# Kernel tuning notes

Measured on AMD Instinct MI355X. Metric: run time of the kernel, lower is better.

The kernel has to match this reference:

```python
import jax, jax.numpy as jnp
import numpy as np

NUM_HEADS = 8
WINDOW = 5


def local_mask(T, w):
    # non-causal band: attend iff |i - j| <= w
    i = jnp.arange(T)
    return jnp.abs(i[:, None] - i[None, :]) <= w


def setup_inputs() -> dict:
    key = jax.random.key(0)
    k1, k2, k3 = jax.random.split(key, 3)
    B, T, S, C = 2, 64, 1024, 512  # batch, frames, spatial (32x32), hidden
    x = jax.random.normal(k1, (B, T * S, C), dtype=jnp.float32)
    W_qkv = jax.random.normal(k2, (C, 3 * C), dtype=jnp.float32) * (C ** -0.5)
    W_out = jax.random.normal(k3, (C, C), dtype=jnp.float32) * (C ** -0.5)
    return {"x": x, "W_qkv": W_qkv, "W_out": W_out, "num_frames": T}


def reference(x, W_qkv, W_out, num_frames):
    B, N, C = x.shape
    H = NUM_HEADS
    hd = C // H
    T = num_frames
    S = N // T
    scale = hd ** -0.5

    qkv = (x @ W_qkv).reshape(B, T, S, 3, H, hd)
    q = qkv[:, :, :, 0]  # [B,T,S,H,hd]
    k = qkv[:, :, :, 1]
    v = qkv[:, :, :, 2]

    # temporal attention: independent per (batch, head, spatial location)
    scores = jnp.einsum('btshd,bushd->bhstu', q, k) * scale  # [B,H,S,T,T]
    mask = local_mask(T, WINDOW)  # [T,T]
    scores = jnp.where(mask[None, None, None], scores, -jnp.inf)
    attn = jax.nn.softmax(scores, axis=-1)
    out = jnp.einsum('bhstu,bushd->btshd', attn, v)  # [B,T,S,H,hd]
    out = out.reshape(B, N, C) @ W_out
    return out
```

## Files before the change

### kernel.cpp

```cpp
#include <hip/hip_runtime.h>
#include <stdint.h>

#define B_   2
#define T_   64
#define S_   1024
#define C_   512
#define H_   8
#define N_   (T_ * S_)
#define M_   (B_ * N_)
#define WIN_ 5

typedef unsigned short u16;
typedef __bf16 bf16;
typedef __bf16 bf16x8 __attribute__((ext_vector_type(8)));
typedef float  f32x4  __attribute__((ext_vector_type(4)));
typedef u16    u16x8  __attribute__((ext_vector_type(8)));

static __device__ __forceinline__ u16 f2bf(float f) {
    return __builtin_bit_cast(u16, (bf16)f);
}
static __device__ __forceinline__ float bf2f(u16 u) {
    return __builtin_bit_cast(float, (uint32_t)u << 16);
}
static __device__ __forceinline__ void gload16(const void* g, void* l) {
    __builtin_amdgcn_global_load_lds(
        (const __attribute__((address_space(1))) void*)g,
        (__attribute__((address_space(3))) void*)l, 16, 0, 0);
}
static __device__ __forceinline__ long permute_row(long grow) {
    int b = (int)(grow >> 16);
    int t = (int)(grow >> 10) & 63;
    int s = (int)grow & 1023;
    return ((long)((b << 10) | s)) * 64 + t;
}


__global__ __launch_bounds__(256) void prep_w(const float* __restrict__ W,
                                              u16* __restrict__ WT, int NCOL) {
    int id = blockIdx.x * 256 + threadIdx.x;
    int n  = id % NCOL;
    int gi = id / NCOL;
    int chunk = gi >> 2;
    int g     = gi & 3;
    int k0 = chunk * 32 + g * 8;
    int cs = chunk ^ ((n >> 3) & 1);
    int gs = g ^ ((n >> 1) & 3);
    u16x8 w;
    #pragma unroll
    for (int j = 0; j < 8; ++j) w[j] = f2bf(W[(size_t)(k0 + j) * NCOL + n]);
    *(u16x8*)&WT[(size_t)n * 512 + cs * 32 + gs * 8] = w;
}

__global__ __launch_bounds__(256) void prep_w2(const float* __restrict__ W,
                                               u16* __restrict__ WT2) {
    int id = blockIdx.x * 256 + threadIdx.x;
    int n  = id % 1536;
    int gi = id / 1536;
    int chunk = gi >> 2;
    int g     = gi & 3;
    int k0 = chunk * 32 + g * 8;
    int which = n >> 9;
    int h     = (n >> 6) & 7;
    int d     = n & 63;
    int rloc  = which * 64 + d;
    long np   = h * 192 + rloc;
    int cs = chunk ^ ((rloc >> 3) & 1);
    int gs = g ^ ((rloc >> 1) & 3);
    u16x8 w;
    #pragma unroll
    for (int j = 0; j < 8; ++j) w[j] = f2bf(W[(size_t)(k0 + j) * 1536 + n]);
    *(u16x8*)&WT2[(size_t)np * 512 + cs * 32 + gs * 8] = w;
}

__global__ __launch_bounds__(256) void prep_x(const float* __restrict__ x,
                                              u16* __restrict__ xb) {
    const size_t total = (size_t)M_ * 64;
    for (size_t id = (size_t)blockIdx.x * 256 + threadIdx.x; id < total;
         id += (size_t)gridDim.x * 256) {
        long r_in = (long)(id >> 6);
        int  gi   = (int)(id & 63);
        int chunk = gi >> 2;
        int g     = gi & 3;
        long rid  = permute_row(r_in);
        int cb  = (int)(rid >> 3) & 1;
        int key = (int)(rid >> 1) & 3;
        const float* src = x + r_in * 512 + chunk * 32 + g * 8;
        f32x4 v0 = *(const f32x4*)(src);
        f32x4 v1 = *(const f32x4*)(src + 4);
        u16x8 w;
        #pragma unroll
        for (int j = 0; j < 4; ++j) { w[j] = f2bf(v0[j]); w[4 + j] = f2bf(v1[j]); }
        *(u16x8*)&xb[(size_t)rid * 512 + (chunk ^ cb) * 32 + ((g ^ key) << 3)] = w;
    }
}

#define LDF(off) __builtin_bit_cast(bf16x8, *(const u16x8*)&lds[(off)])
#define MFMA16(d, a, b) d = __builtin_amdgcn_mfma_f32_16x16x32_bf16(a, b, d, 0, 0, 0)

#define PSTR 200

__global__ __launch_bounds__(512, 4) void gemm_attn(const u16* __restrict__ Ap,
                                                    const u16* __restrict__ Bp,
                                                    u16* __restrict__ attn) {
    __shared__ u16 lds[40960];

    const int tid  = threadIdx.x;
    const int lane = tid & 63;
    const int wid  = tid >> 6;
    const int wm   = wid >> 2;
    const int wn   = wid & 3;
    const int fr   = lane & 15;
    const int g0   = lane >> 4;

    const int rowtile = ((blockIdx.x >> 6) << 3) | (blockIdx.x & 7);
    const int h       = (blockIdx.x >> 3) & 7;
    const long row0   = (long)rowtile * 128;

    int aoffs[4], boffs[3];
    #pragma unroll
    for (int mf = 0; mf < 4; ++mf) {
        int lr = wm * 64 + mf * 16 + fr;
        aoffs[mf] = lr * 64 + (((lr >> 3) & 1) << 5) + (((g0 ^ (lr >> 1)) & 3) << 3);
    }
    #pragma unroll
    for (int nf = 0; nf < 3; ++nf) {
        int lc = wn * 48 + nf * 16 + fr;
        boffs[nf] = lc * 64 + (((lc >> 3) & 1) << 5) + (((g0 ^ (lc >> 1)) & 3) << 3);
    }

    const int srow = lane >> 3;
    const int scol = (lane & 7) * 8;

    auto stageA = [&](int tt, int half) {
        const int ab = (tt & 1) * 8192;
        int r = half * 64 + wid * 8 + srow;
        const u16* g = Ap + (row0 + r) * 512 + tt * 64 + scol;
        gload16(g, (void*)&lds[ab + r * 64]);
    };
    auto stageB = [&](int tt) {
        const int bb = 16384 + (tt & 1) * 12288;
        #pragma unroll
        for (int i = 0; i < 3; ++i) {
            int r = i * 64 + wid * 8 + srow;
            const u16* g = Bp + (size_t)(h * 192 + r) * 512 + tt * 64 + scol;
            gload16(g, (void*)&lds[bb + r * 64]);
        }
    };

    f32x4 acc[4][3] = {};

    stageA(0, 0); stageA(0, 1); stageB(0); stageB(1);
    asm volatile("s_waitcnt vmcnt(3)" ::: "memory");
    __builtin_amdgcn_sched_barrier(0);
    __builtin_amdgcn_s_barrier();

    #pragma unroll
    for (int t = 0; t < 8; ++t) {
        const int ab = (t & 1) * 8192;
        const int bb = 16384 + (t & 1) * 12288;
        bf16x8 af[4], bfv[3];
        #pragma unroll
        for (int mf = 0; mf < 4; ++mf) af[mf] = LDF(ab + aoffs[mf]);
        #pragma unroll
        for (int nf = 0; nf < 3; ++nf) bfv[nf] = LDF(bb + boffs[nf]);
        if (t <= 6) { stageA(t + 1, 0); stageA(t + 1, 1); }
        __builtin_amdgcn_s_barrier();
        asm volatile("s_waitcnt lgkmcnt(0)" ::: "memory");
        __builtin_amdgcn_sched_barrier(0);
        __builtin_amdgcn_s_setprio(1);
        #pragma unroll
        for (int mf = 0; mf < 4; ++mf) {
            MFMA16(acc[mf][0], af[mf], bfv[0]);
            MFMA16(acc[mf][1], af[mf], bfv[1]);
            MFMA16(acc[mf][2], af[mf], bfv[2]);
        }
        __builtin_amdgcn_s_setprio(0);
        __builtin_amdgcn_s_barrier();
        #pragma unroll
        for (int mf = 0; mf < 4; ++mf) af[mf] = LDF(ab + (aoffs[mf] ^ 32));
        #pragma unroll
        for (int nf = 0; nf < 3; ++nf) bfv[nf] = LDF(bb + (boffs[nf] ^ 32));
        __builtin_amdgcn_s_barrier();
        asm volatile("s_waitcnt lgkmcnt(0)" ::: "memory");
        __builtin_amdgcn_sched_barrier(0);
        __builtin_amdgcn_s_setprio(1);
        #pragma unroll
        for (int mf = 0; mf < 4; ++mf) {
            MFMA16(acc[mf][0], af[mf], bfv[0]);
            MFMA16(acc[mf][1], af[mf], bfv[1]);
            MFMA16(acc[mf][2], af[mf], bfv[2]);
        }
        __builtin_amdgcn_s_setprio(0);
        __builtin_amdgcn_s_barrier();
        if (t <= 6) {
            if (t <= 5) {
                stageB(t + 2);
                asm volatile("s_waitcnt vmcnt(3)" ::: "memory");
            } else {
                asm volatile("s_waitcnt vmcnt(0)" ::: "memory");
            }
            __builtin_amdgcn_sched_barrier(0);
            __builtin_amdgcn_s_barrier();
        }
    }

    __builtin_amdgcn_sched_barrier(0);
    #pragma unroll
    for (int mf = 0; mf < 4; ++mf) {
        #pragma unroll
        for (int nf = 0; nf < 3; ++nf) {
            #pragma unroll
            for (int r = 0; r < 4; ++r) {
                int row = wm * 64 + mf * 16 + (lane >> 4) * 4 + r;
                int col = wn * 48 + nf * 16 + fr;
                lds[row * PSTR + col] = f2bf(acc[mf][nf][r]);
            }
        }
    }
    __syncthreads();

    float* scr = (float*)&lds[25600];

    {
        const int slab = wid >> 2;
        const int I    = wid & 3;
        const int abase = (slab * 64 + I * 16 + fr) * PSTR;
        bf16x8 qa0 = LDF(abase + g0 * 8);
        bf16x8 qa1 = LDF(abase + 32 + g0 * 8);
        #pragma unroll
        for (int dj = -1; dj <= 1; ++dj) {
            int J = I + dj;
            if (J >= 0 && J <= 3) {
                const int bbase = (slab * 64 + J * 16 + fr) * PSTR + 64;
                bf16x8 kb0 = LDF(bbase + g0 * 8);
                bf16x8 kb1 = LDF(bbase + 32 + g0 * 8);
                f32x4 sv = {0.f, 0.f, 0.f, 0.f};
                MFMA16(sv, qa0, kb0);
                MFMA16(sv, qa1, kb1);
                #pragma unroll
                for (int r = 0; r < 4; ++r) {
                    int row = I * 16 + (lane >> 4) * 4 + r;
                    int u   = J * 16 + fr;
                    int i   = u - row + WIN_;
                    if (i >= 0 && i < 11)
                        scr[(slab * 64 + row) * 13 + i] = sv[r];
                }
            }
        }
    }
    __syncthreads();

    {
        const int slab = wid >> 2;
        const int q    = wid & 3;
        const int t    = lane;
        const int prow = slab * 64 + t;

        float p[11];
        float m = -1e30f;
        #pragma unroll
        for (int i = 0; i < 11; ++i) {
            int u = t - WIN_ + i;
            if (u >= 0 && u < 64) {
                p[i] = scr[prow * 13 + i] * 0.125f;
                m = fmaxf(m, p[i]);
            } else {
                p[i] = -1e30f;
            }
        }
        float sum = 0.f;
        #pragma unroll
        for (int i = 0; i < 11; ++i) {
            int u = t - WIN_ + i;
            float e = (u >= 0 && u < 64) ? __expf(p[i] - m) : 0.f;
            p[i] = e;
            sum += e;
        }
        const float inv = 1.f / sum;

        float o[16];
        #pragma unroll
        for (int d = 0; d < 16; ++d) o[d] = 0.f;
        #pragma unroll
        for (int i = 0; i < 11; ++i) {
            int u = t - WIN_ + i;
            if (u >= 0 && u < 64) {
                const int ub = (slab * 64 + u) * PSTR + 128;
                float pv = p[i] * inv;
                #pragma unroll
                for (int cc = 0; cc < 2; ++cc) {
                    u16x8 vv = *(const u16x8*)&lds[ub + (q * 2 + cc) * 8];
                    #pragma unroll
                    for (int j = 0; j < 8; ++j) o[cc * 8 + j] += pv * bf2f(vv[j]);
                }
            }
        }
        long rid = row0 + prow;
        int s = (int)(rid >> 6) & 1023;
        size_t rowbase = (size_t)rid * C_;
        const int cb  = (s >> 3) & 1;
        const int key = (s >> 1) & 3;
        #pragma unroll
        for (int cc = 0; cc < 2; ++cc) {
            int c = q * 2 + cc;
            u16x8 w;
            #pragma unroll
            for (int j = 0; j < 8; ++j) w[j] = f2bf(o[cc * 8 + j]);
            int off = (((2 * h + (c >> 2)) ^ cb) << 5) + (((c & 3) ^ key) << 3);
            *(u16x8*)&attn[rowbase + off] = w;
        }
    }
}

template<int NCOL, bool OUT_BF16, bool A_PERM>
__global__ __launch_bounds__(512, 2) void gemm8_k(const u16* __restrict__ Ap,
                                                  const u16* __restrict__ Bp,
                                                  void* __restrict__ Dp, int gx) {
    __shared__ u16 lds[65536];

    const int tid  = threadIdx.x;
    const int lane = tid & 63;
    const int wid  = tid >> 6;
    const int wm   = wid >> 2;
    const int wn   = wid & 3;
    const int fr   = lane & 15;
    const int g0   = lane >> 4;

    const int nwg = gridDim.x;
    const int q8  = nwg >> 3;
    const int bid = blockIdx.x;
    const int wg  = (bid & 7) * q8 + (bid >> 3);
    const int bx  = wg % gx;
    const int by  = wg / gx;
    const long row0 = (long)by * 256;
    const int  col0 = bx * 256;

    int aoffs[8], boffs[4];
    #pragma unroll
    for (int mf = 0; mf < 8; ++mf) {
        int lr = wm * 128 + mf * 16 + fr;
        aoffs[mf] = lr * 64 + (((lr >> 3) & 1) << 5) + (((g0 ^ (lr >> 1)) & 3) << 3);
    }
    #pragma unroll
    for (int nf = 0; nf < 4; ++nf) {
        int lc = wn * 64 + nf * 16 + fr;
        boffs[nf] = lc * 64 + (((lc >> 3) & 1) << 5) + (((g0 ^ (lc >> 1)) & 3) << 3);
    }

    const int srow = lane >> 3;
    const int scol = (lane & 7) * 8;

    long arow_phys[4];
    #pragma unroll
    for (int half = 0; half < 2; ++half)
        #pragma unroll
        for (int i = 0; i < 2; ++i) {
            int r = half * 128 + i * 64 + wid * 8 + srow;
            long grow = row0 + r;
            arow_phys[half * 2 + i] = A_PERM ? permute_row(grow) : grow;
        }

    auto stageA = [&](int tt, int half) {
        const int ab = (tt & 1) * 32768;
        #pragma unroll
        for (int i = 0; i < 2; ++i) {
            int r = half * 128 + i * 64 + wid * 8 + srow;
            const u16* g = Ap + arow_phys[half * 2 + i] * 512 + tt * 64 + scol;
            gload16(g, (void*)&lds[ab + r * 64]);
        }
    };
    auto stageB = [&](int tt, int half) {
        const int ab = (tt & 1) * 32768;
        #pragma unroll
        for (int i = 0; i < 2; ++i) {
            int r = half * 128 + i * 64 + wid * 8 + srow;
            const u16* g = Bp + (size_t)(col0 + r) * 512 + tt * 64 + scol;
            gload16(g, (void*)&lds[ab + 16384 + r * 64]);
        }
    };

    f32x4 acc[8][4] = {};

    stageA(0, 0); stageA(0, 1); stageB(0, 0); stageB(0, 1);
    stageB(1, 0); stageB(1, 1);
    asm volatile("s_waitcnt vmcnt(4)" ::: "memory");
    __builtin_amdgcn_sched_barrier(0);
    __builtin_amdgcn_s_barrier();

    #pragma unroll
    for (int t = 0; t < 8; ++t) {
        const int ab = (t & 1) * 32768;
        bf16x8 af0[8], af1[8], bf0[4], bf1[4];
        #pragma unroll
        for (int mf = 0; mf < 4; ++mf) af0[mf] = LDF(ab + aoffs[mf]);
        #pragma unroll
        for (int nf = 0; nf < 4; ++nf) bf0[nf] = LDF(ab + 16384 + boffs[nf]);
        if (t <= 6) stageA(t + 1, 0);
        __builtin_amdgcn_s_barrier();
        asm volatile("s_waitcnt lgkmcnt(0)" ::: "memory");
        __builtin_amdgcn_sched_barrier(0);
        __builtin_amdgcn_s_setprio(1);
        #pragma unroll
        for (int mf = 0; mf < 4; ++mf) {
            MFMA16(acc[mf][0], af0[mf], bf0[0]);
            MFMA16(acc[mf][1], af0[mf], bf0[1]);
            MFMA16(acc[mf][2], af0[mf], bf0[2]);
            MFMA16(acc[mf][3], af0[mf], bf0[3]);
        }
        __builtin_amdgcn_s_setprio(0);
        __builtin_amdgcn_s_barrier();
        #pragma unroll
        for (int mf = 4; mf < 8; ++mf) af0[mf] = LDF(ab + aoffs[mf]);
        #pragma unroll
        for (int nf = 0; nf < 4; ++nf) bf1[nf] = LDF(ab + 16384 + (boffs[nf] ^ 32));
        if (t <= 6) stageA(t + 1, 1);
        __builtin_amdgcn_s_barrier();
        asm volatile("s_waitcnt lgkmcnt(0)" ::: "memory");
        __builtin_amdgcn_sched_barrier(0);
        __builtin_amdgcn_s_setprio(1);
        #pragma unroll
        for (int mf = 4; mf < 8; ++mf) {
            MFMA16(acc[mf][0], af0[mf], bf0[0]);
            MFMA16(acc[mf][1], af0[mf], bf0[1]);
            MFMA16(acc[mf][2], af0[mf], bf0[2]);
            MFMA16(acc[mf][3], af0[mf], bf0[3]);
        }
        __builtin_amdgcn_s_setprio(0);
        __builtin_amdgcn_s_barrier();
        #pragma unroll
        for (int mf = 0; mf < 4; ++mf) af1[mf] = LDF(ab + (aoffs[mf] ^ 32));
        if (t <= 5) stageB(t + 2, 0);
        __builtin_amdgcn_s_barrier();
        asm volatile("s_waitcnt lgkmcnt(0)" ::: "memory");
        __builtin_amdgcn_sched_barrier(0);
        __builtin_amdgcn_s_setprio(1);
        #pragma unroll
        for (int mf = 0; mf < 4; ++mf) {
            MFMA16(acc[mf][0], af1[mf], bf1[0]);
            MFMA16(acc[mf][1], af1[mf], bf1[1]);
            MFMA16(acc[mf][2], af1[mf], bf1[2]);
            MFMA16(acc[mf][3], af1[mf], bf1[3]);
        }
        __builtin_amdgcn_s_setprio(0);
        __builtin_amdgcn_s_barrier();
        #pragma unroll
        for (int mf = 4; mf < 8; ++mf) af1[mf] = LDF(ab + (aoffs[mf] ^ 32));
        if (t <= 5) stageB(t + 2, 1);
        __builtin_amdgcn_s_barrier();
        asm volatile("s_waitcnt lgkmcnt(0)" ::: "memory");
        __builtin_amdgcn_sched_barrier(0);
        __builtin_amdgcn_s_setprio(1);
        #pragma unroll
        for (int mf = 4; mf < 8; ++mf) {
            MFMA16(acc[mf][0], af1[mf], bf1[0]);
            MFMA16(acc[mf][1], af1[mf], bf1[1]);
            MFMA16(acc[mf][2], af1[mf], bf1[2]);
            MFMA16(acc[mf][3], af1[mf], bf1[3]);
        }
        __builtin_amdgcn_s_setprio(0);
        if (t <= 5) {
            asm volatile("s_waitcnt vmcnt(4)" ::: "memory");
        } else if (t == 6) {
            asm volatile("s_waitcnt vmcnt(0)" ::: "memory");
        }
        __builtin_amdgcn_sched_barrier(0);
        __builtin_amdgcn_s_barrier();
    }

    #pragma unroll
    for (int mf = 0; mf < 8; ++mf) {
        #pragma unroll
        for (int nf = 0; nf < 4; ++nf) {
            #pragma unroll
            for (int r = 0; r < 4; ++r) {
                long grow = row0 + wm * 128 + mf * 16 + (lane >> 4) * 4 + r;
                int  gcol = col0 + wn * 64 + nf * 16 + fr;
                float v = acc[mf][nf][r];
                if constexpr (OUT_BF16) ((u16*)Dp)[grow * NCOL + gcol] = f2bf(v);
                else                    ((float*)Dp)[grow * NCOL + gcol] = v;
            }
        }
    }
}

extern "C" void kernel_launch(void* const* d_in, const int* in_sizes, int n_in,
                              void* d_out, int out_size, void* d_ws, size_t ws_size,
                              hipStream_t stream) {
    const float* x    = (const float*)d_in[0];
    const float* Wqkv = (const float*)d_in[1];
    const float* Wout = (const float*)d_in[2];
    float* out = (float*)d_out;

    const size_t xc_elems = (size_t)M_ * C_;
    u16* xb       = (u16*)d_ws;
    u16* attn_buf = xb + xc_elems;
    u16* WqkvT2   = attn_buf + xc_elems;
    u16* WoutT    = WqkvT2 + (size_t)1536 * 512;
    if (ws_size < ((size_t)(WoutT + (size_t)512 * 512) - (size_t)d_ws)) return;

    prep_w2<<<(1536 * 64) / 256, 256, 0, stream>>>(Wqkv, WqkvT2);
    prep_w<<<(512 * 64) / 256, 256, 0, stream>>>(Wout, WoutT, 512);
    prep_x<<<8192, 256, 0, stream>>>(x, xb);

    gemm_attn<<<8192, 512, 0, stream>>>(xb, WqkvT2, attn_buf);

    gemm8_k<512, false, true><<<1024, 512, 0, stream>>>(attn_buf, WoutT, (void*)out, 2);
}
```

Before: 454.1 us.

## Compute P·V with MFMA using transposed V and zero-padded probability tile in LDS

Replaces the per-thread scalar accumulation of softmax probabilities times V with a bf16 MFMA matmul. V is written transposed into a separate LDS region, and the unnormalized probabilities go into a zeroed 64x64 tile per slab. The MFMA output is staged back through LDS and normalized by the row sum before the global store. This trades the scalar FMA loop for extra LDS traffic, two added barriers, and rounding the probabilities to bf16. It also spends wasted MFMA work on the mostly-zero banded tile.

Result: slower. 477.5 us (+5.1%).

```diff
diff --git a/kernel.cpp b/kernel.cpp
--- a/kernel.cpp
+++ b/kernel.cpp
@@ -97,7 +97,9 @@
 #define LDF(off) __builtin_bit_cast(bf16x8, *(const u16x8*)&lds[(off)])
 #define MFMA16(d, a, b) d = __builtin_amdgcn_mfma_f32_16x16x32_bf16(a, b, d, 0, 0, 0)
 
-#define PSTR 200
+#define QKSTR 136
+#define VTOFF 17408
+#define POFF  26624
 
 __global__ __launch_bounds__(512, 4) void gemm_attn(const u16* __restrict__ Ap,
                                                     const u16* __restrict__ Bp,
@@ -213,25 +215,36 @@
             for (int r = 0; r < 4; ++r) {
                 int row = wm * 64 + mf * 16 + (lane >> 4) * 4 + r;
                 int col = wn * 48 + nf * 16 + fr;
-                lds[row * PSTR + col] = f2bf(acc[mf][nf][r]);
-            }
-        }
+                u16 v = f2bf(acc[mf][nf][r]);
+                if (col < 128) {
+                    lds[row * QKSTR + col] = v;
+                } else {
+                    lds[VTOFF + (row >> 6) * 4608 + (col - 128) * 72 + (row & 63)] = v;
+                }
+            }
+        }
+    }
+    {
+        u16x8 z = {0, 0, 0, 0, 0, 0, 0, 0};
+        *(u16x8*)&lds[POFF + tid * 16]     = z;
+        *(u16x8*)&lds[POFF + tid * 16 + 8] = z;
+        if (tid < 128) *(u16x8*)&lds[POFF + 8192 + tid * 8] = z;
     }
     __syncthreads();
 
-    float* scr = (float*)&lds[25600];
+    float* scr = (float*)&lds[35840];
 
     {
-        const int slab = wid >> 2;
-        const int I    = wid & 3;
-        const int abase = (slab * 64 + I * 16 + fr) * PSTR;
+        const int sl = wid >> 2;
+        const int I  = wid & 3;
+        const int abase = (sl * 64 + I * 16 + fr) * QKSTR;
         bf16x8 qa0 = LDF(abase + g0 * 8);
         bf16x8 qa1 = LDF(abase + 32 + g0 * 8);
         #pragma unroll
         for (int dj = -1; dj <= 1; ++dj) {
             int J = I + dj;
             if (J >= 0 && J <= 3) {
-                const int bbase = (slab * 64 + J * 16 + fr) * PSTR + 64;
+                const int bbase = (sl * 64 + J * 16 + fr) * QKSTR + 64;
                 bf16x8 kb0 = LDF(bbase + g0 * 8);
                 bf16x8 kb1 = LDF(bbase + 32 + g0 * 8);
                 f32x4 sv = {0.f, 0.f, 0.f, 0.f};
@@ -243,19 +256,19 @@
                     int u   = J * 16 + fr;
                     int i   = u - row + WIN_;
                     if (i >= 0 && i < 11)
-                        scr[(slab * 64 + row) * 13 + i] = sv[r];
+                        scr[(sl * 64 + row) * 13 + i] = sv[r];
                 }
             }
         }
     }
     __syncthreads();
 
+    const int slab = wid >> 2;
+    const int q    = wid & 3;
+    const int t    = lane;
+    const int prow = slab * 64 + t;
+    float inv;
     {
-        const int slab = wid >> 2;
-        const int q    = wid & 3;
-        const int t    = lane;
-        const int prow = slab * 64 + t;
-
         float p[11];
         float m = -1e30f;
         #pragma unroll
@@ -276,24 +289,47 @@
             p[i] = e;
             sum += e;
         }
-        const float inv = 1.f / sum;
-
+        inv = 1.f / sum;
+        if (q == 0) {
+            #pragma unroll
+            for (int i = 0; i < 11; ++i) {
+                int u = t - WIN_ + i;
+                if (u >= 0 && u < 64)
+                    lds[POFF + slab * 4608 + t * 72 + u] = f2bf(p[i]);
+            }
+        }
+    }
+    __syncthreads();
+
+    {
+        const int I = q;
+        const int pb = POFF + slab * 4608 + (I * 16 + fr) * 72;
+        bf16x8 pa0 = LDF(pb + g0 * 8);
+        bf16x8 pa1 = LDF(pb + 32 + g0 * 8);
+        #pragma unroll
+        for (int dt = 0; dt < 4; ++dt) {
+            const int vb = VTOFF + slab * 4608 + (dt * 16 + fr) * 72;
+            bf16x8 vb0 = LDF(vb + g0 * 8);
+            bf16x8 vb1 = LDF(vb + 32 + g0 * 8);
+            f32x4 ov = {0.f, 0.f, 0.f, 0.f};
+            MFMA16(ov, pa0, vb0);
+            MFMA16(ov, pa1, vb1);
+            #pragma unroll
+            for (int r = 0; r < 4; ++r) {
+                int row = I * 16 + (lane >> 4) * 4 + r;
+                lds[(slab * 64 + row) * QKSTR + dt * 16 + fr] = f2bf(ov[r]);
+            }
+        }
+    }
+    __syncthreads();
+
+    {
         float o[16];
         #pragma unroll
-        for (int d = 0; d < 16; ++d) o[d] = 0.f;
-        #pragma unroll
-        for (int i = 0; i < 11; ++i) {
-            int u = t - WIN_ + i;
-            if (u >= 0 && u < 64) {
-                const int ub = (slab * 64 + u) * PSTR + 128;
-                float pv = p[i] * inv;
-                #pragma unroll
-                for (int cc = 0; cc < 2; ++cc) {
-                    u16x8 vv = *(const u16x8*)&lds[ub + (q * 2 + cc) * 8];
-                    #pragma unroll
-                    for (int j = 0; j < 8; ++j) o[cc * 8 + j] += pv * bf2f(vv[j]);
-                }
-            }
+        for (int cc = 0; cc < 2; ++cc) {
+            u16x8 v = *(const u16x8*)&lds[prow * QKSTR + q * 16 + cc * 8];
+            #pragma unroll
+            for (int j = 0; j < 8; ++j) o[cc * 8 + j] = bf2f(v[j]) * inv;
         }
         long rid = row0 + prow;
         int s = (int)(rid >> 6) & 1023;
```
